# Kernel optimization log

Hardware: AMD Instinct MI355X
Metric: run time of the kernel (lower is better)

Reference implementation:

```python
import jax, jax.numpy as jnp
import numpy as np

N, SD, HD, CD, AD = 8192, 64, 128, 32, 8  # num_agents, state_dim, hidden_dim, comm_dim, action_dim
NOISE_SCALE = 0.01


def _l2norm(x, axis):
    # F.normalize: x / max(||x||_2, eps), eps=1e-12
    return x / jnp.maximum(jnp.linalg.norm(x, axis=axis, keepdims=True), 1e-12)


def setup_inputs() -> dict:
    key = jax.random.key(0)
    ks = jax.random.split(key, 12)
    def w(k, shape, scale=0.05):
        return jax.random.normal(k, shape, jnp.float32) * scale
    return {
        "states": jax.random.normal(ks[0], (N, SD), jnp.float32),
        "noise": jax.random.normal(ks[1], (N, HD), jnp.float32),
        # ReasoningCore: Linear(SD+CD->HD), ReLU, Linear(HD->HD)
        "W1": w(ks[2], (SD + CD, HD)), "b1": jnp.zeros((HD,), jnp.float32),
        "W2": w(ks[3], (HD, HD)),      "b2": jnp.zeros((HD,), jnp.float32),
        # CommunicationModule encoder: Linear(HD->CD)
        "Wc": w(ks[4], (HD, CD)), "bc": jnp.zeros((CD,), jnp.float32),
        # GNNLayer: Linear(HD->HD)
        "Wg": w(ks[5], (HD, HD)), "bg": jnp.zeros((HD,), jnp.float32),
        # Policy: Linear(HD->AD)
        "Wp": w(ks[6], (HD, AD)), "bp": jnp.zeros((AD,), jnp.float32),
        # Value: Linear(HD->1)
        "Wv": w(ks[7], (HD, 1)), "bv": jnp.zeros((1,), jnp.float32),
        # RoleHead: Linear(HD->3)
        "Wr": w(ks[8], (HD, 3)), "br": jnp.zeros((3,), jnp.float32),
    }


def reference(states, noise, W1, b1, W2, b2, Wc, bc, Wg, bg, Wp, bp, Wv, bv, Wr, br):
    def core(x, comm):
        h = jax.nn.relu(jnp.concatenate([x, comm], axis=-1) @ W1 + b1)  # [N, HD]
        return h @ W2 + b2

    comm0 = jnp.zeros((N, CD), states.dtype)
    H = core(states, comm0)                                   # [N, HD]
    msgs = _l2norm(H @ Wc + bc, axis=1)                       # [N, CD]
    comm = jnp.broadcast_to(msgs.mean(axis=0, keepdims=True), (N, CD))
    H = core(states, comm)                                    # [N, HD]
    adj = jnp.ones((N, N), states.dtype) / N                  # dense uniform adjacency
    H = jax.nn.relu((adj @ H) @ Wg + bg)                      # GNN layer
    H = _l2norm(H + noise * NOISE_SCALE, axis=1)
    actions = jnp.tanh(H @ Wp + bp)                           # [N, AD]
    values = H @ Wv + bv                                      # [N, 1]
    role_probs = jax.nn.softmax(H @ Wr + br, axis=-1)         # [N, 3]
    return (H, actions, values, role_probs)
```

## Files before the change

### kernel.cpp

```cpp
#include <hip/hip_runtime.h>
#include <math.h>

#define N_AG 8192
#define SD 64
#define HD 128
#define CD 32
#define AD 8

#define P_OFF     0
#define W2C_OFF   (N_AG*HD)
#define BCP_OFF   (W2C_OFF + HD*CD)
#define MSUM_OFF  (BCP_OFF + CD)
#define HSUM_OFF  (MSUM_OFF + CD)
#define G_OFF     (HSUM_OFF + HD)

__global__ void k0_pre(const float* __restrict__ W2, const float* __restrict__ b2,
                       const float* __restrict__ Wc, const float* __restrict__ bc,
                       float* __restrict__ ws) {
    float* W2c  = ws + W2C_OFF;
    float* bcp  = ws + BCP_OFF;
    float* msum = ws + MSUM_OFF;
    float* hsum = ws + HSUM_OFF;
    int tid = threadIdx.x;
    if (blockIdx.x < 16) {
        int idx = blockIdx.x * 256 + tid;
        int i = idx >> 5, c = idx & 31;
        float s = 0.f;
        #pragma unroll 8
        for (int k = 0; k < HD; ++k) s += W2[i*HD + k] * Wc[k*CD + c];
        W2c[idx] = s;
    } else {
        if (tid < CD) {
            float s = bc[tid];
            for (int k = 0; k < HD; ++k) s += b2[k] * Wc[k*CD + tid];
            bcp[tid] = s;
            msum[tid] = 0.f;
        }
        if (tid >= 64 && tid < 64 + HD) hsum[tid - 64] = 0.f;
    }
}

#define APB1 16
__global__ void k1_phaseA(const float* __restrict__ X, const float* __restrict__ W1,
                          const float* __restrict__ b1, float* __restrict__ ws) {
    const float* W2c = ws + W2C_OFF;
    const float* bcp = ws + BCP_OFF;
    float* P    = ws + P_OFF;
    float* msum = ws + MSUM_OFF;
    __shared__ float sX[APB1][SD];
    __shared__ float sH[APB1][HD + 1];
    __shared__ float sM[APB1][CD + 1];
    __shared__ float sR[APB1];
    int tid = threadIdx.x;
    int a0 = blockIdx.x * APB1;
    for (int i = tid; i < APB1 * SD; i += 256) sX[i >> 6][i & 63] = X[a0 * SD + i];
    __syncthreads();
    for (int idx = tid; idx < APB1 * HD; idx += 256) {
        int ag = idx >> 7, c = idx & 127;
        float s = b1[c];
        #pragma unroll
        for (int k = 0; k < SD; ++k) s += sX[ag][k] * W1[k*HD + c];
        P[(a0 + ag)*HD + c] = s;
        sH[ag][c] = fmaxf(s, 0.f);
    }
    __syncthreads();
    for (int idx = tid; idx < APB1 * CD; idx += 256) {
        int ag = idx >> 5, c = idx & 31;
        float s = bcp[c];
        #pragma unroll 16
        for (int k = 0; k < HD; ++k) s += sH[ag][k] * W2c[k*CD + c];
        sM[ag][c] = s;
    }
    __syncthreads();
    if (tid < APB1) {
        float ss = 0.f;
        for (int c = 0; c < CD; ++c) { float m = sM[tid][c]; ss += m * m; }
        sR[tid] = 1.f / fmaxf(sqrtf(ss), 1e-12f);
    }
    __syncthreads();
    if (tid < CD) {
        float s = 0.f;
        for (int ag = 0; ag < APB1; ++ag) s += sM[ag][tid] * sR[ag];
        atomicAdd(&msum[tid], s);
    }
}

#define APB2 16
__global__ void k2_phaseB(const float* __restrict__ W1, float* __restrict__ ws) {
    const float* P    = ws + P_OFF;
    const float* msum = ws + MSUM_OFF;
    float* hsum = ws + HSUM_OFF;
    __shared__ float cvec[HD];
    __shared__ float red[256];
    int tid = threadIdx.x;
    if (tid < HD) {
        float s = 0.f;
        #pragma unroll
        for (int k = 0; k < CD; ++k) s += msum[k] * W1[(SD + k)*HD + tid];
        cvec[tid] = s * (1.f / (float)N_AG);
    }
    __syncthreads();
    int c = tid & 127, half = tid >> 7;
    int a0 = blockIdx.x * APB2;
    float part = 0.f;
    for (int ag = half; ag < APB2; ag += 2)
        part += fmaxf(P[(a0 + ag)*HD + c] + cvec[c], 0.f);
    red[tid] = part;
    __syncthreads();
    if (tid < HD) atomicAdd(&hsum[tid], red[tid] + red[tid + 128]);
}

__global__ void k3_gvec(const float* __restrict__ W2, const float* __restrict__ b2,
                        const float* __restrict__ Wg, const float* __restrict__ bg,
                        float* __restrict__ ws) {
    const float* hsum = ws + HSUM_OFF;
    float* g = ws + G_OFF;
    __shared__ float hm[HD];
    __shared__ float u[HD];
    int t = threadIdx.x;
    hm[t] = hsum[t] * (1.f / (float)N_AG);
    __syncthreads();
    float s = b2[t];
    #pragma unroll 16
    for (int k = 0; k < HD; ++k) s += hm[k] * W2[k*HD + t];
    u[t] = s;
    __syncthreads();
    float s2 = bg[t];
    #pragma unroll 16
    for (int k = 0; k < HD; ++k) s2 += u[k] * Wg[k*HD + t];
    g[t] = fmaxf(s2, 0.f);
}

__global__ void k4_out(const float* __restrict__ noise,
                       const float* __restrict__ Wp, const float* __restrict__ bp,
                       const float* __restrict__ Wv, const float* __restrict__ bv,
                       const float* __restrict__ Wr, const float* __restrict__ br,
                       const float* __restrict__ ws, float* __restrict__ out) {
    const float* g = ws + G_OFF;
    int gtid = blockIdx.x * blockDim.x + threadIdx.x;
    int a = gtid >> 6;
    int lane = threadIdx.x & 63;
    if (a >= N_AG) return;
    float v0 = g[lane]      + 0.01f * noise[a*HD + lane];
    float v1 = g[lane + 64] + 0.01f * noise[a*HD + 64 + lane];
    float ss = v0 * v0 + v1 * v1;
    #pragma unroll
    for (int off = 32; off; off >>= 1) ss += __shfl_xor(ss, off);
    float rinv = 1.f / fmaxf(sqrtf(ss), 1e-12f);
    float h0 = v0 * rinv, h1 = v1 * rinv;
    float* outH = out;
    float* outA = out + N_AG * HD;
    float* outV = outA + N_AG * AD;
    float* outR = outV + N_AG;
    outH[a*HD + lane]      = h0;
    outH[a*HD + 64 + lane] = h1;
    float acc[12];
    #pragma unroll
    for (int j = 0; j < 8; ++j)
        acc[j] = h0 * Wp[lane*AD + j] + h1 * Wp[(lane + 64)*AD + j];
    acc[8] = h0 * Wv[lane] + h1 * Wv[lane + 64];
    #pragma unroll
    for (int j = 0; j < 3; ++j)
        acc[9 + j] = h0 * Wr[lane*3 + j] + h1 * Wr[(lane + 64)*3 + j];
    #pragma unroll
    for (int j = 0; j < 12; ++j) {
        #pragma unroll
        for (int off = 32; off; off >>= 1) acc[j] += __shfl_xor(acc[j], off);
    }
    if (lane < 8) {
        outA[a*AD + lane] = tanhf(acc[lane] + bp[lane]);
    } else if (lane == 8) {
        outV[a] = acc[8] + bv[0];
    } else if (lane >= 9 && lane < 12) {
        float l0 = acc[9] + br[0], l1 = acc[10] + br[1], l2 = acc[11] + br[2];
        float m = fmaxf(l0, fmaxf(l1, l2));
        float e0 = expf(l0 - m), e1 = expf(l1 - m), e2 = expf(l2 - m);
        float denom = e0 + e1 + e2;
        float mine = (lane == 9) ? e0 : (lane == 10) ? e1 : e2;
        outR[a*3 + (lane - 9)] = mine / denom;
    }
}

extern "C" void kernel_launch(void* const* d_in, const int* in_sizes, int n_in,
                              void* d_out, int out_size, void* d_ws, size_t ws_size,
                              hipStream_t stream) {
    const float* states = (const float*)d_in[0];
    const float* noise  = (const float*)d_in[1];
    const float* W1 = (const float*)d_in[2];
    const float* b1 = (const float*)d_in[3];
    const float* W2 = (const float*)d_in[4];
    const float* b2 = (const float*)d_in[5];
    const float* Wc = (const float*)d_in[6];
    const float* bc = (const float*)d_in[7];
    const float* Wg = (const float*)d_in[8];
    const float* bg = (const float*)d_in[9];
    const float* Wp = (const float*)d_in[10];
    const float* bp = (const float*)d_in[11];
    const float* Wv = (const float*)d_in[12];
    const float* bv = (const float*)d_in[13];
    const float* Wr = (const float*)d_in[14];
    const float* br = (const float*)d_in[15];
    float* ws  = (float*)d_ws;
    float* out = (float*)d_out;

    hipLaunchKernelGGL(k0_pre,   dim3(17),           dim3(256), 0, stream, W2, b2, Wc, bc, ws);
    hipLaunchKernelGGL(k1_phaseA,dim3(N_AG / APB1),  dim3(256), 0, stream, states, W1, b1, ws);
    hipLaunchKernelGGL(k2_phaseB,dim3(N_AG / APB2),  dim3(256), 0, stream, W1, ws);
    hipLaunchKernelGGL(k3_gvec,  dim3(1),            dim3(128), 0, stream, W2, b2, Wg, bg, ws);
    hipLaunchKernelGGL(k4_out,   dim3(N_AG / 4),     dim3(256), 0, stream, noise, Wp, bp, Wv, bv, Wr, br, ws, out);
}
```

Baseline: 142.1 us.

## Fuse all phases into one cooperative kernel with grid syncs

Replaces the five-kernel pipeline with a single cooperative kernel of 512 blocks that uses grid.sync between the message-mean, hidden-mean and output phases. Per-block intermediates (P, hidden activations) stay in shared memory instead of round-tripping through global workspace. The message sum becomes per-block partials reduced after the sync, replacing global atomics. The W2·Wc precompute is dropped in favor of computing W2 then Wc per block, which adds redundant FLOPs. The approach also depends on all 512 blocks being co-resident for the cooperative launch.

```diff
diff --git a/kernel.cpp b/kernel.cpp
--- a/kernel.cpp
+++ b/kernel.cpp
@@ -1,183 +1,216 @@
 #include <hip/hip_runtime.h>
+#include <hip/hip_cooperative_groups.h>
 #include <math.h>
+
+namespace cg = cooperative_groups;
 
 #define N_AG 8192
 #define SD 64
 #define HD 128
 #define CD 32
 #define AD 8
-
-#define P_OFF     0
-#define W2C_OFF   (N_AG*HD)
-#define BCP_OFF   (W2C_OFF + HD*CD)
-#define MSUM_OFF  (BCP_OFF + CD)
-#define HSUM_OFF  (MSUM_OFF + CD)
-#define G_OFF     (HSUM_OFF + HD)
-
-__global__ void k0_pre(const float* __restrict__ W2, const float* __restrict__ b2,
-                       const float* __restrict__ Wc, const float* __restrict__ bc,
-                       float* __restrict__ ws) {
-    float* W2c  = ws + W2C_OFF;
-    float* bcp  = ws + BCP_OFF;
-    float* msum = ws + MSUM_OFF;
-    float* hsum = ws + HSUM_OFF;
-    int tid = threadIdx.x;
-    if (blockIdx.x < 16) {
-        int idx = blockIdx.x * 256 + tid;
-        int i = idx >> 5, c = idx & 31;
-        float s = 0.f;
-        #pragma unroll 8
-        for (int k = 0; k < HD; ++k) s += W2[i*HD + k] * Wc[k*CD + c];
-        W2c[idx] = s;
-    } else {
-        if (tid < CD) {
-            float s = bc[tid];
-            for (int k = 0; k < HD; ++k) s += b2[k] * Wc[k*CD + tid];
-            bcp[tid] = s;
-            msum[tid] = 0.f;
-        }
-        if (tid >= 64 && tid < 64 + HD) hsum[tid - 64] = 0.f;
-    }
-}
-
-#define APB1 16
-__global__ void k1_phaseA(const float* __restrict__ X, const float* __restrict__ W1,
-                          const float* __restrict__ b1, float* __restrict__ ws) {
-    const float* W2c = ws + W2C_OFF;
-    const float* bcp = ws + BCP_OFF;
-    float* P    = ws + P_OFF;
-    float* msum = ws + MSUM_OFF;
-    __shared__ float sX[APB1][SD];
-    __shared__ float sH[APB1][HD + 1];
-    __shared__ float sM[APB1][CD + 1];
-    __shared__ float sR[APB1];
-    int tid = threadIdx.x;
-    int a0 = blockIdx.x * APB1;
-    for (int i = tid; i < APB1 * SD; i += 256) sX[i >> 6][i & 63] = X[a0 * SD + i];
-    __syncthreads();
-    for (int idx = tid; idx < APB1 * HD; idx += 256) {
-        int ag = idx >> 7, c = idx & 127;
-        float s = b1[c];
-        #pragma unroll
-        for (int k = 0; k < SD; ++k) s += sX[ag][k] * W1[k*HD + c];
-        P[(a0 + ag)*HD + c] = s;
-        sH[ag][c] = fmaxf(s, 0.f);
-    }
-    __syncthreads();
-    for (int idx = tid; idx < APB1 * CD; idx += 256) {
-        int ag = idx >> 5, c = idx & 31;
-        float s = bcp[c];
-        #pragma unroll 16
-        for (int k = 0; k < HD; ++k) s += sH[ag][k] * W2c[k*CD + c];
-        sM[ag][c] = s;
-    }
-    __syncthreads();
-    if (tid < APB1) {
+#define NBLK 512
+#define APB 16
+
+#define MPARTS_OFF 0
+#define HSUM_OFF   (NBLK * CD)
+
+__global__ __launch_bounds__(256, 2)
+void fused_mas(const float* __restrict__ X, const float* __restrict__ noise,
+               const float* __restrict__ W1, const float* __restrict__ b1,
+               const float* __restrict__ W2, const float* __restrict__ b2,
+               const float* __restrict__ Wc, const float* __restrict__ bc,
+               const float* __restrict__ Wg, const float* __restrict__ bg,
+               const float* __restrict__ Wp, const float* __restrict__ bp,
+               const float* __restrict__ Wv, const float* __restrict__ bv,
+               const float* __restrict__ Wr, const float* __restrict__ br,
+               float* __restrict__ ws, float* __restrict__ out)
+{
+    cg::grid_group grid = cg::this_grid();
+    __shared__ float sX[APB][SD];
+    __shared__ float sP[APB][HD];
+    __shared__ float sT[APB][HD];
+    __shared__ float sU[APB][HD];
+    __shared__ float sM[APB][CD + 1];
+    __shared__ float sR[APB];
+    __shared__ float sMsum[CD];
+    __shared__ float sVec[HD];
+    __shared__ float sVec2[HD];
+    __shared__ float sRed[256];
+
+    const int tid = threadIdx.x;
+    const int b = blockIdx.x;
+    const int a0 = b * APB;
+
+    for (int i = tid; i < APB * SD; i += 256)
+        sX[i >> 6][i & 63] = X[a0 * SD + i];
+    if (b == 0 && tid < HD) ws[HSUM_OFF + tid] = 0.f;
+    __syncthreads();
+
+    {
+        const int c = tid & 127;
+        const int ag0 = tid >> 7;
+        float acc[8];
+        #pragma unroll
+        for (int i = 0; i < 8; ++i) acc[i] = b1[c];
+        for (int k = 0; k < SD; ++k) {
+            float w = W1[k * HD + c];
+            #pragma unroll
+            for (int i = 0; i < 8; ++i) acc[i] += sX[ag0 + 2 * i][k] * w;
+        }
+        #pragma unroll
+        for (int i = 0; i < 8; ++i) {
+            int ag = ag0 + 2 * i;
+            sP[ag][c] = acc[i];
+            sT[ag][c] = fmaxf(acc[i], 0.f);
+        }
+    }
+    __syncthreads();
+    {
+        const int c = tid & 127;
+        const int ag0 = tid >> 7;
+        float acc[8];
+        #pragma unroll
+        for (int i = 0; i < 8; ++i) acc[i] = b2[c];
+        for (int k = 0; k < HD; ++k) {
+            float w = W2[k * HD + c];
+            #pragma unroll
+            for (int i = 0; i < 8; ++i) acc[i] += sT[ag0 + 2 * i][k] * w;
+        }
+        #pragma unroll
+        for (int i = 0; i < 8; ++i) sU[ag0 + 2 * i][c] = acc[i];
+    }
+    __syncthreads();
+    {
+        const int c = tid & 31;
+        const int ag0 = tid >> 5;
+        float acc0 = bc[c], acc1 = bc[c];
+        for (int k = 0; k < HD; ++k) {
+            float w = Wc[k * CD + c];
+            acc0 += sU[ag0][k] * w;
+            acc1 += sU[ag0 + 8][k] * w;
+        }
+        sM[ag0][c] = acc0;
+        sM[ag0 + 8][c] = acc1;
+    }
+    __syncthreads();
+    if (tid < APB) {
         float ss = 0.f;
-        for (int c = 0; c < CD; ++c) { float m = sM[tid][c]; ss += m * m; }
+        #pragma unroll
+        for (int c2 = 0; c2 < CD; ++c2) { float m = sM[tid][c2]; ss += m * m; }
         sR[tid] = 1.f / fmaxf(sqrtf(ss), 1e-12f);
     }
     __syncthreads();
     if (tid < CD) {
         float s = 0.f;
-        for (int ag = 0; ag < APB1; ++ag) s += sM[ag][tid] * sR[ag];
-        atomicAdd(&msum[tid], s);
-    }
-}
-
-#define APB2 16
-__global__ void k2_phaseB(const float* __restrict__ W1, float* __restrict__ ws) {
-    const float* P    = ws + P_OFF;
-    const float* msum = ws + MSUM_OFF;
-    float* hsum = ws + HSUM_OFF;
-    __shared__ float cvec[HD];
-    __shared__ float red[256];
-    int tid = threadIdx.x;
+        #pragma unroll
+        for (int ag = 0; ag < APB; ++ag) s += sM[ag][tid] * sR[ag];
+        ws[MPARTS_OFF + b * CD + tid] = s;
+    }
+    grid.sync();
+
+    {
+        const int c = tid & 31, chunk = tid >> 5;
+        float s = 0.f;
+        for (int p = chunk * 64; p < chunk * 64 + 64; ++p)
+            s += ws[MPARTS_OFF + p * CD + c];
+        sRed[tid] = s;
+    }
+    __syncthreads();
+    if (tid < CD) {
+        float s = 0.f;
+        #pragma unroll
+        for (int j = 0; j < 8; ++j) s += sRed[j * 32 + tid];
+        sMsum[tid] = s;
+    }
+    __syncthreads();
     if (tid < HD) {
         float s = 0.f;
         #pragma unroll
-        for (int k = 0; k < CD; ++k) s += msum[k] * W1[(SD + k)*HD + tid];
-        cvec[tid] = s * (1.f / (float)N_AG);
-    }
-    __syncthreads();
-    int c = tid & 127, half = tid >> 7;
-    int a0 = blockIdx.x * APB2;
-    float part = 0.f;
-    for (int ag = half; ag < APB2; ag += 2)
-        part += fmaxf(P[(a0 + ag)*HD + c] + cvec[c], 0.f);
-    red[tid] = part;
-    __syncthreads();
-    if (tid < HD) atomicAdd(&hsum[tid], red[tid] + red[tid + 128]);
-}
-
-__global__ void k3_gvec(const float* __restrict__ W2, const float* __restrict__ b2,
-                        const float* __restrict__ Wg, const float* __restrict__ bg,
-                        float* __restrict__ ws) {
-    const float* hsum = ws + HSUM_OFF;
-    float* g = ws + G_OFF;
-    __shared__ float hm[HD];
-    __shared__ float u[HD];
-    int t = threadIdx.x;
-    hm[t] = hsum[t] * (1.f / (float)N_AG);
-    __syncthreads();
-    float s = b2[t];
-    #pragma unroll 16
-    for (int k = 0; k < HD; ++k) s += hm[k] * W2[k*HD + t];
-    u[t] = s;
-    __syncthreads();
-    float s2 = bg[t];
-    #pragma unroll 16
-    for (int k = 0; k < HD; ++k) s2 += u[k] * Wg[k*HD + t];
-    g[t] = fmaxf(s2, 0.f);
-}
-
-__global__ void k4_out(const float* __restrict__ noise,
-                       const float* __restrict__ Wp, const float* __restrict__ bp,
-                       const float* __restrict__ Wv, const float* __restrict__ bv,
-                       const float* __restrict__ Wr, const float* __restrict__ br,
-                       const float* __restrict__ ws, float* __restrict__ out) {
-    const float* g = ws + G_OFF;
-    int gtid = blockIdx.x * blockDim.x + threadIdx.x;
-    int a = gtid >> 6;
-    int lane = threadIdx.x & 63;
-    if (a >= N_AG) return;
-    float v0 = g[lane]      + 0.01f * noise[a*HD + lane];
-    float v1 = g[lane + 64] + 0.01f * noise[a*HD + 64 + lane];
-    float ss = v0 * v0 + v1 * v1;
+        for (int k = 0; k < CD; ++k) s += sMsum[k] * W1[(SD + k) * HD + tid];
+        sVec[tid] = s * (1.f / (float)N_AG);
+    }
+    __syncthreads();
+    {
+        const int c = tid & 127, half = tid >> 7;
+        float part = 0.f;
+        #pragma unroll
+        for (int ag = half; ag < APB; ag += 2)
+            part += fmaxf(sP[ag][c] + sVec[c], 0.f);
+        sRed[tid] = part;
+    }
+    __syncthreads();
+    if (tid < HD) atomicAdd(&ws[HSUM_OFF + tid], sRed[tid] + sRed[tid + 128]);
+    grid.sync();
+
+    if (tid < HD) sVec2[tid] = ws[HSUM_OFF + tid] * (1.f / (float)N_AG);
+    __syncthreads();
+    if (tid < HD) {
+        float s = b2[tid];
+        for (int k = 0; k < HD; ++k) s += sVec2[k] * W2[k * HD + tid];
+        sVec[tid] = s;
+    }
+    __syncthreads();
+    if (tid < HD) {
+        float s = bg[tid];
+        for (int k = 0; k < HD; ++k) s += sVec[k] * Wg[k * HD + tid];
+        sVec2[tid] = fmaxf(s, 0.f);
+    }
+    __syncthreads();
+
+    const int lane = tid & 63;
+    const int w = tid >> 6;
+    float wp0[AD], wp1[AD];
     #pragma unroll
-    for (int off = 32; off; off >>= 1) ss += __shfl_xor(ss, off);
-    float rinv = 1.f / fmaxf(sqrtf(ss), 1e-12f);
-    float h0 = v0 * rinv, h1 = v1 * rinv;
+    for (int j = 0; j < AD; ++j) { wp0[j] = Wp[lane * AD + j]; wp1[j] = Wp[(lane + 64) * AD + j]; }
+    float wv0 = Wv[lane], wv1 = Wv[lane + 64];
+    float wr0[3], wr1[3];
+    #pragma unroll
+    for (int j = 0; j < 3; ++j) { wr0[j] = Wr[lane * 3 + j]; wr1[j] = Wr[(lane + 64) * 3 + j]; }
+    const float g0 = sVec2[lane], g1 = sVec2[lane + 64];
+    const float bpl = (lane < AD) ? bp[lane] : 0.f;
+    const float bv0 = bv[0];
+    const float br0 = br[0], br1 = br[1], br2 = br[2];
+
     float* outH = out;
     float* outA = out + N_AG * HD;
     float* outV = outA + N_AG * AD;
     float* outR = outV + N_AG;
-    outH[a*HD + lane]      = h0;
-    outH[a*HD + 64 + lane] = h1;
-    float acc[12];
-    #pragma unroll
-    for (int j = 0; j < 8; ++j)
-        acc[j] = h0 * Wp[lane*AD + j] + h1 * Wp[(lane + 64)*AD + j];
-    acc[8] = h0 * Wv[lane] + h1 * Wv[lane + 64];
-    #pragma unroll
-    for (int j = 0; j < 3; ++j)
-        acc[9 + j] = h0 * Wr[lane*3 + j] + h1 * Wr[(lane + 64)*3 + j];
-    #pragma unroll
-    for (int j = 0; j < 12; ++j) {
-        #pragma unroll
-        for (int off = 32; off; off >>= 1) acc[j] += __shfl_xor(acc[j], off);
-    }
-    if (lane < 8) {
-        outA[a*AD + lane] = tanhf(acc[lane] + bp[lane]);
-    } else if (lane == 8) {
-        outV[a] = acc[8] + bv[0];
-    } else if (lane >= 9 && lane < 12) {
-        float l0 = acc[9] + br[0], l1 = acc[10] + br[1], l2 = acc[11] + br[2];
-        float m = fmaxf(l0, fmaxf(l1, l2));
-        float e0 = expf(l0 - m), e1 = expf(l1 - m), e2 = expf(l2 - m);
-        float denom = e0 + e1 + e2;
-        float mine = (lane == 9) ? e0 : (lane == 10) ? e1 : e2;
-        outR[a*3 + (lane - 9)] = mine / denom;
+
+    for (int ag = w; ag < APB; ag += 4) {
+        int a = a0 + ag;
+        float v0 = g0 + 0.01f * noise[a * HD + lane];
+        float v1 = g1 + 0.01f * noise[a * HD + 64 + lane];
+        float ss = v0 * v0 + v1 * v1;
+        #pragma unroll
+        for (int off = 32; off; off >>= 1) ss += __shfl_xor(ss, off);
+        float rinv = 1.f / fmaxf(sqrtf(ss), 1e-12f);
+        float h0 = v0 * rinv, h1 = v1 * rinv;
+        outH[a * HD + lane]      = h0;
+        outH[a * HD + 64 + lane] = h1;
+        float acc[12];
+        #pragma unroll
+        for (int j = 0; j < AD; ++j) acc[j] = h0 * wp0[j] + h1 * wp1[j];
+        acc[8] = h0 * wv0 + h1 * wv1;
+        #pragma unroll
+        for (int j = 0; j < 3; ++j) acc[9 + j] = h0 * wr0[j] + h1 * wr1[j];
+        #pragma unroll
+        for (int j = 0; j < 12; ++j) {
+            #pragma unroll
+            for (int off = 32; off; off >>= 1) acc[j] += __shfl_xor(acc[j], off);
+        }
+        if (lane < AD) {
+            outA[a * AD + lane] = tanhf(acc[lane] + bpl);
+        } else if (lane == 8) {
+            outV[a] = acc[8] + bv0;
+        } else if (lane >= 9 && lane < 12) {
+            float l0 = acc[9] + br0, l1 = acc[10] + br1, l2 = acc[11] + br2;
+            float m = fmaxf(l0, fmaxf(l1, l2));
+            float e0 = expf(l0 - m), e1 = expf(l1 - m), e2 = expf(l2 - m);
+            float denom = e0 + e1 + e2;
+            float mine = (lane == 9) ? e0 : (lane == 10) ? e1 : e2;
+            outR[a * 3 + (lane - 9)] = mine / denom;
+        }
     }
 }
 
@@ -203,9 +236,12 @@
     float* ws  = (float*)d_ws;
     float* out = (float*)d_out;
 
-    hipLaunchKernelGGL(k0_pre,   dim3(17),           dim3(256), 0, stream, W2, b2, Wc, bc, ws);
-    hipLaunchKernelGGL(k1_phaseA,dim3(N_AG / APB1),  dim3(256), 0, stream, states, W1, b1, ws);
-    hipLaunchKernelGGL(k2_phaseB,dim3(N_AG / APB2),  dim3(256), 0, stream, W1, ws);
-    hipLaunchKernelGGL(k3_gvec,  dim3(1),            dim3(128), 0, stream, W2, b2, Wg, bg, ws);
-    hipLaunchKernelGGL(k4_out,   dim3(N_AG / 4),     dim3(256), 0, stream, noise, Wp, bp, Wv, bv, Wr, br, ws, out);
+    void* args[] = {
+        (void*)&states, (void*)&noise,
+        (void*)&W1, (void*)&b1, (void*)&W2, (void*)&b2,
+        (void*)&Wc, (void*)&bc, (void*)&Wg, (void*)&bg,
+        (void*)&Wp, (void*)&bp, (void*)&Wv, (void*)&bv,
+        (void*)&Wr, (void*)&br, (void*)&ws, (void*)&out
+    };
+    hipLaunchCooperativeKernel((void*)fused_mas, dim3(NBLK), dim3(256), args, 0, stream);
 }
```

Result: slower. 239.9 us (+68.8%).
